# Optimization experiments

Hardware: AMD Instinct MI355X
Metric: run time of the kernel (lower is better)

The kernel has to match this reference:

```python
import jax, jax.numpy as jnp
import numpy as np

B, T, C, H = 2, 2048, 2048, 16
HD = C // H      # 128 head dim
P = C // 8       # 256 octonion component width
NEG_INF = jnp.finfo(jnp.float32).min

# Cayley octonion multiplication table: e_i * e_j = OCT_SIGN[i,j] * e_{OCT_IDX[i,j]}
OCT_SIGN = np.array([
    [1, 1, 1, 1, 1, 1, 1, 1],
    [1,-1, 1,-1, 1,-1,-1, 1],
    [1,-1,-1, 1, 1, 1,-1,-1],
    [1, 1,-1,-1, 1,-1, 1,-1],
    [1,-1,-1,-1,-1, 1, 1, 1],
    [1, 1,-1, 1,-1,-1,-1, 1],
    [1, 1, 1,-1,-1, 1,-1,-1],
    [1,-1, 1, 1,-1,-1, 1,-1]], dtype=np.float32)
OCT_IDX = np.array([
    [0,1,2,3,4,5,6,7],
    [1,0,3,2,5,4,7,6],
    [2,3,0,1,6,7,4,5],
    [3,2,1,0,7,6,5,4],
    [4,5,6,7,0,1,2,3],
    [5,4,7,6,1,0,3,2],
    [6,7,4,5,2,3,0,1],
    [7,6,5,4,3,2,1,0]], dtype=np.int32)
_comb = np.zeros((8, 8, 8), np.float32)
for _i in range(8):
    for _j in range(8):
        _comb[OCT_IDX[_i, _j], _i, _j] = OCT_SIGN[_i, _j]
COMB = jnp.asarray(_comb)  # (k, i, j): out_k += sign * (W_i @ x_j)


def ternary(W):
    # BitNet-style ternary quantization with straight-through estimator
    s = jnp.mean(jnp.abs(W)) + 1e-8
    q = jnp.round(jnp.clip(W / s, -1.0, 1.0)) * s
    return W + jax.lax.stop_gradient(q - W)


def oct_linear(x, W):
    # x: (B,T,C), W: (8,P,P) -> (B,T,C)
    parts = jnp.stack(jnp.split(x, 8, axis=-1), axis=0)  # (8,B,T,P)
    Wq = ternary(W)
    prod = jnp.einsum('jbtp,ipq->ijbtq', parts, Wq)       # (8,8,B,T,P)
    out = jnp.einsum('kij,ijbtq->kbtq', COMB, prod)       # (8,B,T,P)
    return jnp.transpose(out, (1, 2, 0, 3)).reshape(x.shape[0], x.shape[1], C)


def rope(x, cos, sin):
    # x: (B,T,H,HD); cos/sin: (T, HD//2). Interleaved complex pairs as in view_as_complex.
    xr = x[..., 0::2]
    xi = x[..., 1::2]
    c = cos[None, :x.shape[1], None, :]
    s = sin[None, :x.shape[1], None, :]
    out = jnp.stack([xr * c - xi * s, xr * s + xi * c], axis=-1)
    return out.reshape(x.shape)


def setup_inputs() -> dict:
    key = jax.random.key(0)
    ks = jax.random.split(key, 5)
    x = jax.random.normal(ks[0], (B, T, C), dtype=jnp.float32)
    wq = jax.random.normal(ks[1], (8, P, P), dtype=jnp.float32) * 0.02
    wk = jax.random.normal(ks[2], (8, P, P), dtype=jnp.float32) * 0.02
    wv = jax.random.normal(ks[3], (8, P, P), dtype=jnp.float32) * 0.02
    wo = jax.random.normal(ks[4], (8, P, P), dtype=jnp.float32) * 0.02
    inv = 1.0 / (10000.0 ** (np.arange(0, HD, 2, dtype=np.float32) / HD))
    ang = np.outer(np.arange(T, dtype=np.float32), inv)
    freqs_cos = jnp.asarray(np.cos(ang), dtype=jnp.float32)
    freqs_sin = jnp.asarray(np.sin(ang), dtype=jnp.float32)
    return {"x": x, "wq": wq, "wk": wk, "wv": wv, "wo": wo,
            "freqs_cos": freqs_cos, "freqs_sin": freqs_sin}


def reference(x, wq, wk, wv, wo, freqs_cos, freqs_sin):
    b, t, _ = x.shape
    q = oct_linear(x, wq).reshape(b, t, H, HD)
    k = oct_linear(x, wk).reshape(b, t, H, HD)
    v = oct_linear(x, wv).reshape(b, t, H, HD)
    q = rope(q, freqs_cos, freqs_sin)
    k = rope(k, freqs_cos, freqs_sin)
    q = jnp.transpose(q, (0, 2, 1, 3))  # (B,H,T,HD)
    k = jnp.transpose(k, (0, 2, 1, 3))
    v = jnp.transpose(v, (0, 2, 1, 3))
    scores = jnp.einsum('bhtd,bhsd->bhts', q, k) / jnp.sqrt(jnp.float32(HD))
    mask = jnp.tril(jnp.ones((t, t), dtype=bool))
    scores = jnp.where(mask[None, None], scores, NEG_INF)
    attn = jax.nn.softmax(scores, axis=-1)
    y = jnp.einsum('bhts,bhsd->bhtd', attn, v)
    y = jnp.transpose(y, (0, 2, 1, 3)).reshape(b, t, C)
    return oct_linear(y, wo)
```

## Files before the change

kernel.cpp:

```cpp
#include <hip/hip_runtime.h>


typedef __attribute__((ext_vector_type(8))) short short8;
typedef __attribute__((ext_vector_type(4))) float f32x4;
typedef unsigned short u16;
typedef unsigned int u32;

__device__ __forceinline__ float bf2f(u16 u) {
    u32 x = ((u32)u) << 16;
    return __builtin_bit_cast(float, x);
}
__device__ __forceinline__ u16 f2bf(float f) {
    u32 x = __builtin_bit_cast(u32, f);
    x += 0x7fffu + ((x >> 16) & 1u);
    return (u16)(x >> 16);
}
__device__ __forceinline__ u16 f2bf_trunc(float f) {
    return (u16)(__builtin_bit_cast(u32, f) >> 16);
}
__device__ __forceinline__ u32 pack2(u16 a, u16 b) { return (u32)a | ((u32)b << 16); }

__device__ __forceinline__ void async16(const void* g, void* l) {
    __builtin_amdgcn_global_load_lds((const __attribute__((address_space(1))) u32*)g,
                                     (__attribute__((address_space(3))) u32*)l, 16, 0, 0);
}

__device__ const int d_OCT_IDX[8][8] = {
    {0,1,2,3,4,5,6,7},{1,0,3,2,5,4,7,6},{2,3,0,1,6,7,4,5},{3,2,1,0,7,6,5,4},
    {4,5,6,7,0,1,2,3},{5,4,7,6,1,0,3,2},{6,7,4,5,2,3,0,1},{7,6,5,4,3,2,1,0}};
__device__ const float d_OCT_SIGN[8][8] = {
    { 1, 1, 1, 1, 1, 1, 1, 1},{ 1,-1, 1,-1, 1,-1,-1, 1},{ 1,-1,-1, 1, 1, 1,-1,-1},
    { 1, 1,-1,-1, 1,-1, 1,-1},{ 1,-1,-1,-1,-1, 1, 1, 1},{ 1, 1,-1, 1,-1,-1,-1, 1},
    { 1, 1, 1,-1,-1, 1,-1,-1},{ 1,-1, 1, 1,-1,-1, 1,-1}};

__global__ __launch_bounds__(256) void reduce1_kernel(
    const float* __restrict__ w0, const float* __restrict__ w1,
    const float* __restrict__ w2, const float* __restrict__ w3,
    float* __restrict__ partials) {
    int bid = blockIdx.x, wsel = bid >> 6, part = bid & 63;
    const float* W = wsel == 0 ? w0 : wsel == 1 ? w1 : wsel == 2 ? w2 : w3;
    int base = part * 8192 + threadIdx.x;
    float acc = 0.f;
#pragma unroll
    for (int k = 0; k < 32; k++) acc += fabsf(W[base + k * 256]);
#pragma unroll
    for (int off = 1; off < 64; off <<= 1) acc += __shfl_xor(acc, off, 64);
    __shared__ float r4[4];
    if ((threadIdx.x & 63) == 0) r4[threadIdx.x >> 6] = acc;
    __syncthreads();
    if (threadIdx.x == 0) partials[bid] = r4[0] + r4[1] + r4[2] + r4[3];
}
__global__ __launch_bounds__(256) void reduce2_kernel(const float* __restrict__ partials,
                                                      float* __restrict__ s_vals) {
    int w = threadIdx.x >> 6, lane = threadIdx.x & 63;
    float v = partials[w * 64 + lane];
#pragma unroll
    for (int off = 1; off < 64; off <<= 1) v += __shfl_xor(v, off, 64);
    if (lane == 0) s_vals[w] = v / 524288.0f + 1e-8f;
}

__global__ __launch_bounds__(256) void cast_bf16_kernel(const float* __restrict__ X, u16* __restrict__ Xb) {
    int gid = blockIdx.x * 256 + threadIdx.x;
    const float4* X4 = (const float4*)X;
    float4 a = X4[gid * 2], b = X4[gid * 2 + 1];
    uint4 o;
    o.x = pack2(f2bf(a.x), f2bf(a.y));
    o.y = pack2(f2bf(a.z), f2bf(a.w));
    o.z = pack2(f2bf(b.x), f2bf(b.y));
    o.w = pack2(f2bf(b.z), f2bf(b.w));
    *(uint4*)&Xb[gid * 8] = o;
}

__global__ __launch_bounds__(256) void build_weff_kernel(
    const float* __restrict__ W, const float* __restrict__ sptr, u16* __restrict__ WT) {
    __shared__ float Tt[64 * 68];
    int tid = threadIdx.x;
    int combo = blockIdx.x >> 4, sub = blockIdx.x & 15;
    int j = combo >> 3, kblk = combo & 7;
    int i = 0;
#pragma unroll
    for (int ii = 0; ii < 8; ii++)
        if (d_OCT_IDX[ii][j] == kblk) i = ii;
    float sign = d_OCT_SIGN[i][j];
    int p0 = (sub >> 2) * 64, q0 = (sub & 3) * 64;
    float inv_s = 1.0f / (*sptr);
#pragma unroll
    for (int pass = 0; pass < 4; pass++) {
        int p = p0 + pass * 16 + (tid >> 4);
        int q = q0 + (tid & 15) * 4;
        float4 wv = *(const float4*)&W[i * 65536 + p * 256 + q];
        float* Tp = &Tt[(pass * 16 + (tid >> 4)) * 68 + (tid & 15) * 4];
        Tp[0] = sign * rintf(fminf(1.f, fmaxf(-1.f, wv.x * inv_s)));
        Tp[1] = sign * rintf(fminf(1.f, fmaxf(-1.f, wv.y * inv_s)));
        Tp[2] = sign * rintf(fminf(1.f, fmaxf(-1.f, wv.z * inv_s)));
        Tp[3] = sign * rintf(fminf(1.f, fmaxf(-1.f, wv.w * inv_s)));
    }
    __syncthreads();
#pragma unroll
    for (int pass = 0; pass < 2; pass++) {
        int qq = pass * 32 + (tid >> 3);
        int pl = (tid & 7) * 8;
        u16 r[8];
#pragma unroll
        for (int l = 0; l < 8; l++) r[l] = f2bf_trunc(Tt[(pl + l) * 68 + qq]);
        uint4 o;
        o.x = pack2(r[0], r[1]); o.y = pack2(r[2], r[3]);
        o.z = pack2(r[4], r[5]); o.w = pack2(r[6], r[7]);
        *(uint4*)&WT[(size_t)(kblk * 256 + q0 + qq) * 2048 + j * 256 + p0 + pl] = o;
    }
}

template <int MODE>
__global__ __launch_bounds__(256) void gemm_kernel(
    const u16* __restrict__ A, const u16* __restrict__ Bt,
    const float* __restrict__ sptr, void* __restrict__ Cout) {
    __shared__ __align__(16) u16 As[128 * 32];
    __shared__ __align__(16) u16 Bs[128 * 32];
    const int K = 2048;
    int tid = threadIdx.x, lane = tid & 63, wid = tid >> 6;
    int quad = lane >> 4, l16 = lane & 15;
    int wm = (wid >> 1) * 64, wn = (wid & 1) * 64;
    int m0 = blockIdx.y * 128, n0 = blockIdx.x * 128;
    f32x4 acc[4][4];
#pragma unroll
    for (int a = 0; a < 4; a++)
#pragma unroll
        for (int b = 0; b < 4; b++) acc[a][b] = (f32x4){0.f, 0.f, 0.f, 0.f};
    int srow = lane >> 2;
    int sblk = (lane & 3) ^ (srow & 3);
    const u16* Ag = A + (size_t)(m0 + wid * 32 + srow) * K + sblk * 8;
    const u16* Bg = Bt + (size_t)(n0 + wid * 32 + srow) * K + sblk * 8;
    u16* Al = &As[(wid * 32) * 32];
    u16* Bl = &Bs[(wid * 32) * 32];
    int rblk = (quad ^ (l16 & 3)) * 8;
    for (int k0 = 0; k0 < K; k0 += 32) {
        __syncthreads();
        async16(Ag + k0, Al);
        async16(Ag + k0 + (size_t)16 * K, Al + 16 * 32);
        async16(Bg + k0, Bl);
        async16(Bg + k0 + (size_t)16 * K, Bl + 16 * 32);
        __syncthreads();
        short8 af[4], bfv[4];
#pragma unroll
        for (int mt = 0; mt < 4; mt++) af[mt] = *(const short8*)&As[(wm + mt * 16 + l16) * 32 + rblk];
#pragma unroll
        for (int nt = 0; nt < 4; nt++) bfv[nt] = *(const short8*)&Bs[(wn + nt * 16 + l16) * 32 + rblk];
#pragma unroll
        for (int mt = 0; mt < 4; mt++)
#pragma unroll
            for (int nt = 0; nt < 4; nt++)
                acc[mt][nt] = __builtin_amdgcn_mfma_f32_16x16x32_bf16(af[mt], bfv[nt], acc[mt][nt], 0, 0, 0);
    }
    float s = *sptr;
#pragma unroll
    for (int mt = 0; mt < 4; mt++)
#pragma unroll
        for (int nt = 0; nt < 4; nt++) {
            int mg = m0 + wm + mt * 16 + quad * 4;
            int ng = n0 + wn + nt * 16 + l16;
            if (MODE == 0) {
#pragma unroll
                for (int r = 0; r < 4; r++)
                    ((u16*)Cout)[(size_t)(mg + r) * 2048 + ng] = f2bf(acc[mt][nt][r] * s);
            } else if (MODE == 1) {
#pragma unroll
                for (int r = 0; r < 4; r++)
                    ((float*)Cout)[(size_t)(mg + r) * 2048 + ng] = acc[mt][nt][r] * s;
            } else {
                ushort4 o4;
                o4.x = f2bf(acc[mt][nt][0] * s);
                o4.y = f2bf(acc[mt][nt][1] * s);
                o4.z = f2bf(acc[mt][nt][2] * s);
                o4.w = f2bf(acc[mt][nt][3] * s);
                *(ushort4*)&((u16*)Cout)[((size_t)((mg >> 11) * 16 + (ng >> 7)) * 128 + (ng & 127)) * 2048 + (mg & 2047)] = o4;
            }
        }
}

__global__ __launch_bounds__(256) void rope_kernel(
    u16* __restrict__ Xb, const float* __restrict__ fc, const float* __restrict__ fs, float scale) {
    int gid = blockIdx.x * 256 + threadIdx.x;
    int c2 = gid & 1023;
    int t = (gid >> 10) & 2047;
    int m = c2 & 63;
    u32 u = ((u32*)Xb)[gid];
    float xr = bf2f((u16)(u & 0xffff));
    float xi = bf2f((u16)(u >> 16));
    float c = fc[t * 64 + m] * scale, s = fs[t * 64 + m] * scale;
    ((u32*)Xb)[gid] = pack2(f2bf(xr * c - xi * s), f2bf(xr * s + xi * c));
}

__global__ __launch_bounds__(512, 2) void flash_kernel(
    const u16* __restrict__ Q, const u16* __restrict__ Kg,
    const u16* __restrict__ VTg, u16* __restrict__ Y) {
    __shared__ __align__(16) u16 Ks[2][64 * 128];
    __shared__ __align__(16) u16 Vs[2][128 * 64];
    __shared__ __align__(16) u16 Ps[8 * 16 * 64];
    const int NIT = 34;
    int tid = threadIdx.x, lane = tid & 63, wid = tid >> 6;
    int quad = lane >> 4, l16 = lane & 15;
    int bh = blockIdx.x, b = bh >> 4, h = bh & 15;
    int qt = blockIdx.y;
    int nitA = 2 * qt + 2;
    const u16* Qb = Q + (size_t)b * 2048 * 2048 + h * 128;
    const u16* Kb = Kg + (size_t)b * 2048 * 2048 + h * 128;
    const u16* Vb = VTg + (size_t)bh * 128 * 2048;
    int q0 = qt * 128, nit = nitA;
    int ksr = lane >> 4, ksb = lane & 15;
    int vsr = lane >> 3, vsb = lane & 7;
#pragma unroll
    for (int cc = 0; cc < 2; cc++) {
        int ch = wid * 2 + cc;
        int kr = ch * 4 + ksr;
        async16(&Kb[(size_t)kr * 2048 + (ksb ^ (kr & 15)) * 8], &Ks[0][ch * 512]);
        int vd = ch * 8 + vsr;
        async16(&Vb[(size_t)vd * 2048 + (vsb ^ (vd & 7)) * 8], &Vs[0][ch * 512]);
    }
    short8 qf[4];
#pragma unroll
    for (int kt = 0; kt < 4; kt++)
        qf[kt] = *(const short8*)&Qb[(size_t)(q0 + wid * 16 + l16) * 2048 + kt * 32 + quad * 8];
    f32x4 o[8];
#pragma unroll
    for (int nt = 0; nt < 8; nt++) o[nt] = (f32x4){0.f, 0.f, 0.f, 0.f};
    float m_[4] = {-1e30f, -1e30f, -1e30f, -1e30f};
    float l_[4] = {0.f, 0.f, 0.f, 0.f};
    int il = 0;
    for (int g = 0; g < NIT; g++) {
        int c = g & 1;
        __syncthreads();
        if (g + 1 < NIT) {
            int gn = g + 1;
            int s0n = (gn < nitA ? gn : gn - nitA) * 64;
#pragma unroll
            for (int cc = 0; cc < 2; cc++) {
                int ch = wid * 2 + cc;
                int kr = ch * 4 + ksr;
                async16(&Kb[(size_t)(s0n + kr) * 2048 + (ksb ^ (kr & 15)) * 8], &Ks[1 - c][ch * 512]);
                int vd = ch * 8 + vsr;
                async16(&Vb[(size_t)vd * 2048 + s0n + (vsb ^ (vd & 7)) * 8], &Vs[1 - c][ch * 512]);
            }
        }
        int s0 = il * 64;
        f32x4 sc[4];
#pragma unroll
        for (int ct = 0; ct < 4; ct++) {
            f32x4 a = (f32x4){0.f, 0.f, 0.f, 0.f};
#pragma unroll
            for (int kt = 0; kt < 4; kt++) {
                short8 bfv = *(const short8*)&Ks[c][(ct * 16 + l16) * 128 + ((kt * 4 + quad) ^ l16) * 8];
                a = __builtin_amdgcn_mfma_f32_16x16x32_bf16(qf[kt], bfv, a, 0, 0, 0);
            }
            sc[ct] = a;
        }
        if (il >= nit - 2) {
#pragma unroll
            for (int ct = 0; ct < 4; ct++) {
                int colg = s0 + ct * 16 + l16;
#pragma unroll
                for (int r = 0; r < 4; r++) {
                    int rowg = q0 + wid * 16 + quad * 4 + r;
                    if (colg > rowg) sc[ct][r] = -1e30f;
                }
            }
        }
        float alpha[4];
#pragma unroll
        for (int r = 0; r < 4; r++) {
            float mx = fmaxf(fmaxf(sc[0][r], sc[1][r]), fmaxf(sc[2][r], sc[3][r]));
#pragma unroll
            for (int off = 1; off < 16; off <<= 1) mx = fmaxf(mx, __shfl_xor(mx, off, 64));
            float mn = fmaxf(m_[r], mx);
            float al = exp2f(m_[r] - mn);
            float rs = 0.f;
#pragma unroll
            for (int ct = 0; ct < 4; ct++) {
                float p = exp2f(sc[ct][r] - mn);
                sc[ct][r] = p;
                rs += p;
            }
#pragma unroll
            for (int off = 1; off < 16; off <<= 1) rs += __shfl_xor(rs, off, 64);
            m_[r] = mn;
            l_[r] = l_[r] * al + rs;
            alpha[r] = al;
        }
        u16* Pw = &Ps[wid * 1024];
#pragma unroll
        for (int ct = 0; ct < 4; ct++)
#pragma unroll
            for (int r = 0; r < 4; r++) {
                int lr = quad * 4 + r;
                int key = ct * 16 + l16;
                Pw[lr * 64 + ((key >> 3) ^ (lr & 7)) * 8 + (key & 7)] = f2bf_trunc(sc[ct][r]);
            }
#pragma unroll
        for (int nt = 0; nt < 8; nt++)
#pragma unroll
            for (int r = 0; r < 4; r++) o[nt][r] *= alpha[r];
#pragma unroll
        for (int kt2 = 0; kt2 < 2; kt2++) {
            short8 pa = *(const short8*)&Pw[l16 * 64 + ((kt2 * 4 + quad) ^ (l16 & 7)) * 8];
#pragma unroll
            for (int nt = 0; nt < 8; nt++) {
                short8 vb = *(const short8*)&Vs[c][(nt * 16 + l16) * 64 + ((kt2 * 4 + quad) ^ (l16 & 7)) * 8];
                o[nt] = __builtin_amdgcn_mfma_f32_16x16x32_bf16(pa, vb, o[nt], 0, 0, 0);
            }
        }
        il++;
        if (il == nit && g + 1 < NIT) {
            float iv[4];
#pragma unroll
            for (int r = 0; r < 4; r++) iv[r] = 1.f / l_[r];
#pragma unroll
            for (int nt = 0; nt < 8; nt++)
#pragma unroll
                for (int r = 0; r < 4; r++) {
                    int t_ = q0 + wid * 16 + quad * 4 + r;
                    Y[((size_t)(b * 2048 + t_)) * 2048 + h * 128 + nt * 16 + l16] = f2bf(o[nt][r] * iv[r]);
                }
            q0 = (15 - qt) * 128;
            nit = NIT - nitA;
            il = 0;
#pragma unroll
            for (int kt = 0; kt < 4; kt++)
                qf[kt] = *(const short8*)&Qb[(size_t)(q0 + wid * 16 + l16) * 2048 + kt * 32 + quad * 8];
#pragma unroll
            for (int nt = 0; nt < 8; nt++) o[nt] = (f32x4){0.f, 0.f, 0.f, 0.f};
#pragma unroll
            for (int r = 0; r < 4; r++) { m_[r] = -1e30f; l_[r] = 0.f; }
        }
    }
    float iv[4];
#pragma unroll
    for (int r = 0; r < 4; r++) iv[r] = 1.f / l_[r];
#pragma unroll
    for (int nt = 0; nt < 8; nt++)
#pragma unroll
        for (int r = 0; r < 4; r++) {
            int t_ = q0 + wid * 16 + quad * 4 + r;
            Y[((size_t)(b * 2048 + t_)) * 2048 + h * 128 + nt * 16 + l16] = f2bf(o[nt][r] * iv[r]);
        }
}

extern "C" void kernel_launch(void* const* d_in, const int* in_sizes, int n_in,
                              void* d_out, int out_size, void* d_ws, size_t ws_size,
                              hipStream_t stream) {
    const float* x  = (const float*)d_in[0];
    const float* wq = (const float*)d_in[1];
    const float* wk = (const float*)d_in[2];
    const float* wv = (const float*)d_in[3];
    const float* wo = (const float*)d_in[4];
    const float* fc = (const float*)d_in[5];
    const float* fs = (const float*)d_in[6];
    float* out = (float*)d_out;

    char* ws = (char*)d_ws;
    float* s_vals   = (float*)ws;
    float* partials = (float*)(ws + 1024);
    u16* WT  = (u16*)(ws + 8192);
    u16* xb  = (u16*)(ws + 8192 + 8388608);
    u16* Qb  = xb + 8388608;
    u16* Kb  = Qb + 8388608;
    u16* VTb = Kb + 8388608;

    const float QSCALE = 0.08838834764831845f * 1.4426950408889634f;

    reduce1_kernel<<<256, 256, 0, stream>>>(wq, wk, wv, wo, partials);
    reduce2_kernel<<<1, 256, 0, stream>>>(partials, s_vals);
    cast_bf16_kernel<<<4096, 256, 0, stream>>>(x, xb);

    build_weff_kernel<<<1024, 256, 0, stream>>>(wq, s_vals + 0, WT);
    gemm_kernel<0><<<dim3(16, 32), 256, 0, stream>>>(xb, WT, s_vals + 0, Qb);
    rope_kernel<<<16384, 256, 0, stream>>>(Qb, fc, fs, QSCALE);

    build_weff_kernel<<<1024, 256, 0, stream>>>(wk, s_vals + 1, WT);
    gemm_kernel<0><<<dim3(16, 32), 256, 0, stream>>>(xb, WT, s_vals + 1, Kb);
    rope_kernel<<<16384, 256, 0, stream>>>(Kb, fc, fs, 1.0f);

    build_weff_kernel<<<1024, 256, 0, stream>>>(wv, s_vals + 2, WT);
    gemm_kernel<2><<<dim3(16, 32), 256, 0, stream>>>(xb, WT, s_vals + 2, VTb);

    flash_kernel<<<dim3(32, 8), 512, 0, stream>>>(Qb, Kb, VTb, Qb );

    build_weff_kernel<<<1024, 256, 0, stream>>>(wo, s_vals + 3, WT);
    gemm_kernel<1><<<dim3(16, 32), 256, 0, stream>>>(Qb, WT, s_vals + 3, (void*)out);
}
```

Before: 414.6 us.

## Double-buffer GEMM loads, fuse RoPE into GEMM epilogue, shrink flash tiles

The GEMM main loop now double-buffers its LDS tiles, so the next K-slice is loaded asynchronously while MFMAs run on the current one. That removes one barrier per iteration. RoPE is folded into the Q/K GEMM epilogue using a lane shuffle to pair real and imaginary parts, which removes two separate elementwise kernels and their memory round trips. The flash kernel moves from 512-thread blocks over 128-row query tiles to 256-thread blocks over 64-row tiles, paired for causal balancing, which doubles the grid and applies the mask only on the diagonal block. In exchange, the GEMM uses twice the LDS, the epilogue adds scattered loads of the cos/sin tables, and the flash kernel reloads K/V more often.

```diff
diff --git a/kernel.cpp b/kernel.cpp
--- a/kernel.cpp
+++ b/kernel.cpp
@@ -113,9 +113,10 @@
 template <int MODE>
 __global__ __launch_bounds__(256) void gemm_kernel(
     const u16* __restrict__ A, const u16* __restrict__ Bt,
-    const float* __restrict__ sptr, void* __restrict__ Cout) {
-    __shared__ __align__(16) u16 As[128 * 32];
-    __shared__ __align__(16) u16 Bs[128 * 32];
+    const float* __restrict__ sptr, const float* __restrict__ fc,
+    const float* __restrict__ fs, float rscale, void* __restrict__ Cout) {
+    __shared__ __align__(16) u16 As[2][128 * 32];
+    __shared__ __align__(16) u16 Bs[2][128 * 32];
     const int K = 2048;
     int tid = threadIdx.x, lane = tid & 63, wid = tid >> 6;
     int quad = lane >> 4, l16 = lane & 15;
@@ -130,27 +131,31 @@
     int sblk = (lane & 3) ^ (srow & 3);
     const u16* Ag = A + (size_t)(m0 + wid * 32 + srow) * K + sblk * 8;
     const u16* Bg = Bt + (size_t)(n0 + wid * 32 + srow) * K + sblk * 8;
-    u16* Al = &As[(wid * 32) * 32];
-    u16* Bl = &Bs[(wid * 32) * 32];
     int rblk = (quad ^ (l16 & 3)) * 8;
-    for (int k0 = 0; k0 < K; k0 += 32) {
+#define GSTAGE(k0_, buf_)                                              \
+    do {                                                               \
+        async16(Ag + (k0_), &As[buf_][wid * 1024]);                    \
+        async16(Ag + (k0_) + (size_t)16 * K, &As[buf_][wid * 1024 + 512]); \
+        async16(Bg + (k0_), &Bs[buf_][wid * 1024]);                    \
+        async16(Bg + (k0_) + (size_t)16 * K, &Bs[buf_][wid * 1024 + 512]); \
+    } while (0)
+    GSTAGE(0, 0);
+    for (int it = 0; it < K / 32; it++) {
+        int c = it & 1;
         __syncthreads();
-        async16(Ag + k0, Al);
-        async16(Ag + k0 + (size_t)16 * K, Al + 16 * 32);
-        async16(Bg + k0, Bl);
-        async16(Bg + k0 + (size_t)16 * K, Bl + 16 * 32);
-        __syncthreads();
+        if (it + 1 < K / 32) GSTAGE((it + 1) * 32, 1 - c);
         short8 af[4], bfv[4];
 #pragma unroll
-        for (int mt = 0; mt < 4; mt++) af[mt] = *(const short8*)&As[(wm + mt * 16 + l16) * 32 + rblk];
-#pragma unroll
-        for (int nt = 0; nt < 4; nt++) bfv[nt] = *(const short8*)&Bs[(wn + nt * 16 + l16) * 32 + rblk];
+        for (int mt = 0; mt < 4; mt++) af[mt] = *(const short8*)&As[c][(wm + mt * 16 + l16) * 32 + rblk];
+#pragma unroll
+        for (int nt = 0; nt < 4; nt++) bfv[nt] = *(const short8*)&Bs[c][(wn + nt * 16 + l16) * 32 + rblk];
 #pragma unroll
         for (int mt = 0; mt < 4; mt++)
 #pragma unroll
             for (int nt = 0; nt < 4; nt++)
                 acc[mt][nt] = __builtin_amdgcn_mfma_f32_16x16x32_bf16(af[mt], bfv[nt], acc[mt][nt], 0, 0, 0);
     }
+#undef GSTAGE
     float s = *sptr;
 #pragma unroll
     for (int mt = 0; mt < 4; mt++)
@@ -159,9 +164,20 @@
             int mg = m0 + wm + mt * 16 + quad * 4;
             int ng = n0 + wn + nt * 16 + l16;
             if (MODE == 0) {
-#pragma unroll
-                for (int r = 0; r < 4; r++)
-                    ((u16*)Cout)[(size_t)(mg + r) * 2048 + ng] = f2bf(acc[mt][nt][r] * s);
+                int mi = (ng & 127) >> 1;
+#pragma unroll
+                for (int r = 0; r < 4; r++) {
+                    float v = acc[mt][nt][r] * s;
+                    float vp = __shfl_xor(v, 1, 64);
+                    int t = mg + r;
+                    int tm = t & 2047;
+                    float cs = fc[tm * 64 + mi] * rscale;
+                    float sn = fs[tm * 64 + mi] * rscale;
+                    if (!(ng & 1)) {
+                        u32 pk = pack2(f2bf(v * cs - vp * sn), f2bf(v * sn + vp * cs));
+                        ((u32*)Cout)[((size_t)t * 2048 + ng) >> 1] = pk;
+                    }
+                }
             } else if (MODE == 1) {
 #pragma unroll
                 for (int r = 0; r < 4; r++)
@@ -177,44 +193,31 @@
         }
 }
 
-__global__ __launch_bounds__(256) void rope_kernel(
-    u16* __restrict__ Xb, const float* __restrict__ fc, const float* __restrict__ fs, float scale) {
-    int gid = blockIdx.x * 256 + threadIdx.x;
-    int c2 = gid & 1023;
-    int t = (gid >> 10) & 2047;
-    int m = c2 & 63;
-    u32 u = ((u32*)Xb)[gid];
-    float xr = bf2f((u16)(u & 0xffff));
-    float xi = bf2f((u16)(u >> 16));
-    float c = fc[t * 64 + m] * scale, s = fs[t * 64 + m] * scale;
-    ((u32*)Xb)[gid] = pack2(f2bf(xr * c - xi * s), f2bf(xr * s + xi * c));
-}
-
-__global__ __launch_bounds__(512, 2) void flash_kernel(
+__global__ __launch_bounds__(256, 2) void flash_kernel(
     const u16* __restrict__ Q, const u16* __restrict__ Kg,
     const u16* __restrict__ VTg, u16* __restrict__ Y) {
     __shared__ __align__(16) u16 Ks[2][64 * 128];
     __shared__ __align__(16) u16 Vs[2][128 * 64];
-    __shared__ __align__(16) u16 Ps[8 * 16 * 64];
-    const int NIT = 34;
+    __shared__ __align__(16) u16 Ps[4 * 16 * 64];
+    const int NIT = 33;
     int tid = threadIdx.x, lane = tid & 63, wid = tid >> 6;
     int quad = lane >> 4, l16 = lane & 15;
     int bh = blockIdx.x, b = bh >> 4, h = bh & 15;
-    int qt = blockIdx.y;
-    int nitA = 2 * qt + 2;
+    int pr = blockIdx.y;
+    int nitA = pr + 1;
     const u16* Qb = Q + (size_t)b * 2048 * 2048 + h * 128;
     const u16* Kb = Kg + (size_t)b * 2048 * 2048 + h * 128;
     const u16* Vb = VTg + (size_t)bh * 128 * 2048;
-    int q0 = qt * 128, nit = nitA;
-    int ksr = lane >> 4, ksb = lane & 15;
-    int vsr = lane >> 3, vsb = lane & 7;
-#pragma unroll
-    for (int cc = 0; cc < 2; cc++) {
-        int ch = wid * 2 + cc;
-        int kr = ch * 4 + ksr;
-        async16(&Kb[(size_t)kr * 2048 + (ksb ^ (kr & 15)) * 8], &Ks[0][ch * 512]);
-        int vd = ch * 8 + vsr;
-        async16(&Vb[(size_t)vd * 2048 + (vsb ^ (vd & 7)) * 8], &Vs[0][ch * 512]);
+    int q0 = pr * 64, nit = nitA;
+    int krow = lane >> 4, kblk = lane & 15;
+    int vrow = lane >> 3, vblk = lane & 7;
+#pragma unroll
+    for (int cc = 0; cc < 4; cc++) {
+        int ch = wid * 4 + cc;
+        int kr = ch * 4 + krow;
+        async16(&Kb[(size_t)kr * 2048 + (kblk ^ (kr & 15)) * 8], &Ks[0][ch * 512]);
+        int vd = ch * 8 + vrow;
+        async16(&Vb[(size_t)vd * 2048 + (vblk ^ (vd & 7)) * 8], &Vs[0][ch * 512]);
     }
     short8 qf[4];
 #pragma unroll
@@ -233,12 +236,12 @@
             int gn = g + 1;
             int s0n = (gn < nitA ? gn : gn - nitA) * 64;
 #pragma unroll
-            for (int cc = 0; cc < 2; cc++) {
-                int ch = wid * 2 + cc;
-                int kr = ch * 4 + ksr;
-                async16(&Kb[(size_t)(s0n + kr) * 2048 + (ksb ^ (kr & 15)) * 8], &Ks[1 - c][ch * 512]);
-                int vd = ch * 8 + vsr;
-                async16(&Vb[(size_t)vd * 2048 + s0n + (vsb ^ (vd & 7)) * 8], &Vs[1 - c][ch * 512]);
+            for (int cc = 0; cc < 4; cc++) {
+                int ch = wid * 4 + cc;
+                int kr = ch * 4 + krow;
+                async16(&Kb[(size_t)(s0n + kr) * 2048 + (kblk ^ (kr & 15)) * 8], &Ks[1 - c][ch * 512]);
+                int vd = ch * 8 + vrow;
+                async16(&Vb[(size_t)vd * 2048 + s0n + (vblk ^ (vd & 7)) * 8], &Vs[1 - c][ch * 512]);
             }
         }
         int s0 = il * 64;
@@ -253,7 +256,7 @@
             }
             sc[ct] = a;
         }
-        if (il >= nit - 2) {
+        if (il == nit - 1) {
 #pragma unroll
             for (int ct = 0; ct < 4; ct++) {
                 int colg = s0 + ct * 16 + l16;
@@ -319,7 +322,7 @@
                     int t_ = q0 + wid * 16 + quad * 4 + r;
                     Y[((size_t)(b * 2048 + t_)) * 2048 + h * 128 + nt * 16 + l16] = f2bf(o[nt][r] * iv[r]);
                 }
-            q0 = (15 - qt) * 128;
+            q0 = (31 - pr) * 64;
             nit = NIT - nitA;
             il = 0;
 #pragma unroll
@@ -371,18 +374,16 @@
     cast_bf16_kernel<<<4096, 256, 0, stream>>>(x, xb);
 
     build_weff_kernel<<<1024, 256, 0, stream>>>(wq, s_vals + 0, WT);
-    gemm_kernel<0><<<dim3(16, 32), 256, 0, stream>>>(xb, WT, s_vals + 0, Qb);
-    rope_kernel<<<16384, 256, 0, stream>>>(Qb, fc, fs, QSCALE);
+    gemm_kernel<0><<<dim3(16, 32), 256, 0, stream>>>(xb, WT, s_vals + 0, fc, fs, QSCALE, Qb);
 
     build_weff_kernel<<<1024, 256, 0, stream>>>(wk, s_vals + 1, WT);
-    gemm_kernel<0><<<dim3(16, 32), 256, 0, stream>>>(xb, WT, s_vals + 1, Kb);
-    rope_kernel<<<16384, 256, 0, stream>>>(Kb, fc, fs, 1.0f);
+    gemm_kernel<0><<<dim3(16, 32), 256, 0, stream>>>(xb, WT, s_vals + 1, fc, fs, 1.0f, Kb);
 
     build_weff_kernel<<<1024, 256, 0, stream>>>(wv, s_vals + 2, WT);
-    gemm_kernel<2><<<dim3(16, 32), 256, 0, stream>>>(xb, WT, s_vals + 2, VTb);
-
-    flash_kernel<<<dim3(32, 8), 512, 0, stream>>>(Qb, Kb, VTb, Qb );
+    gemm_kernel<2><<<dim3(16, 32), 256, 0, stream>>>(xb, WT, s_vals + 2, fc, fs, 0.f, VTb);
+
+    flash_kernel<<<dim3(32, 16), 256, 0, stream>>>(Qb, Kb, VTb, Qb );
 
     build_weff_kernel<<<1024, 256, 0, stream>>>(wo, s_vals + 3, WT);
-    gemm_kernel<1><<<dim3(16, 32), 256, 0, stream>>>(Qb, WT, s_vals + 3, (void*)out);
-}
+    gemm_kernel<1><<<dim3(16, 32), 256, 0, stream>>>(Qb, WT, s_vals + 3, fc, fs, 0.f, (void*)out);
+}
```

Result: slower. 454.9 us (+9.7%).
